# Performance work log

Measured on AMD Instinct MI355X. Metric: run time of the kernel, lower is better.

Reference implementation:

```python
import jax, jax.numpy as jnp
import numpy as np

ARITY, LABEL_DIM, H_DIM, B = 2, 128, 512, 16384
ARG_DIM = LABEL_DIM + ARITY * H_DIM


def setup_inputs() -> dict:
    key = jax.random.key(0)
    ks = jax.random.split(key, 12)
    s_lin = 1.0 / np.sqrt(ARG_DIM)
    inp = {
        "label": jax.random.normal(ks[0], (B, LABEL_DIM), jnp.float32),
        "children_h": jax.random.normal(ks[1], (ARITY, B, H_DIM), jnp.float32),
        "children_c": jax.random.normal(ks[2], (ARITY, B, H_DIM), jnp.float32),
        # torch Linear params: W (h, arg_dim), b (h,)
        "W_i": jax.random.normal(ks[3], (H_DIM, ARG_DIM), jnp.float32) * s_lin,
        "b_i": jax.random.normal(ks[4], (H_DIM,), jnp.float32) * s_lin,
        "W_o": jax.random.normal(ks[5], (H_DIM, ARG_DIM), jnp.float32) * s_lin,
        "b_o": jax.random.normal(ks[6], (H_DIM,), jnp.float32) * s_lin,
        "W_u": jax.random.normal(ks[7], (H_DIM, ARG_DIM), jnp.float32) * s_lin,
        "b_u": jax.random.normal(ks[8], (H_DIM,), jnp.float32) * s_lin,
        # forget params (xavier-ish init)
        "W_fl": jax.random.normal(ks[9], (H_DIM, LABEL_DIM), jnp.float32) * np.sqrt(2.0 / (H_DIM + LABEL_DIM)),
        "W_fs": jax.random.normal(ks[10], (ARITY, ARITY, H_DIM, H_DIM), jnp.float32) * np.sqrt(1.0 / H_DIM),
        "forget_bias": jax.random.normal(ks[11], (H_DIM,), jnp.float32) * 0.1,
    }
    return inp


def reference(label, children_h, children_c, W_i, b_i, W_o, b_o, W_u, b_u, W_fl, W_fs, forget_bias):
    arity, b, h = children_h.shape
    # x = cat([label, h_0, ..., h_{arity-1}], dim=1)  -> (B, arg_dim)
    x = jnp.concatenate([label, children_h.transpose(1, 0, 2).reshape(b, arity * h)], axis=1)
    i_gate = jax.nn.sigmoid(x @ W_i.T + b_i)
    o_gate = jax.nn.sigmoid(x @ W_o.T + b_o)
    u = jnp.tanh(x @ W_u.T + b_u)
    # per-child forget weight: [W_fl | W_fs[k,0] | ... | W_fs[k,arity-1]]  -> (arity, h, arg_dim)
    Wf = jnp.concatenate(
        [jnp.broadcast_to(W_fl, (arity,) + W_fl.shape),
         W_fs.transpose(0, 2, 1, 3).reshape(arity, h, arity * h)],
        axis=2,
    )
    # bmm (no bias inside sigmoid; forget_bias enters separately below)
    f = jax.nn.sigmoid(jnp.einsum("khd,bd->kbh", Wf, x))
    cells_composed = (f * children_c).sum(axis=0)          # (B, h)
    cells_forget_bias = forget_bias * children_c.sum(axis=0)
    next_cell = i_gate * u + cells_composed + cells_forget_bias
    out = jnp.tanh(o_gate * next_cell)
    return (next_cell, out)
```

## Files before the change

### kernel.cpp

```cpp
#include <hip/hip_runtime.h>
#include <hip/hip_bf16.h>
#include <cstdint>
#include <cstddef>

#define BROWS   16384
#define LDIM    128
#define HDIM    512
#define KDIM    1152
#define NGATES  2560

#define XB_BYTES  ((size_t)BROWS * KDIM * 2)
#define WB_BYTES  ((size_t)NGATES * KDIM * 2)

using f32x4   = __attribute__((ext_vector_type(4))) float;
using bfrag   = __attribute__((ext_vector_type(8))) short;

__device__ __forceinline__ short f2bf(float f) {
    union { float f; uint32_t u; } a; a.f = f;
    uint32_t u = a.u;
    uint32_t lsb = (u >> 16) & 1u;
    u += 0x7fffu + lsb;
    return (short)(u >> 16);
}
__device__ __forceinline__ float bf2f(short s) {
    union { uint32_t u; float f; } a;
    a.u = ((uint32_t)(uint16_t)s) << 16;
    return a.f;
}

__device__ __forceinline__ void load_lds16(const void* g, void* l) {
    __builtin_amdgcn_global_load_lds(
        (const __attribute__((address_space(1))) void*)g,
        (__attribute__((address_space(3))) void*)l, 16, 0, 0);
}

__device__ __forceinline__ float fast_sigmoid(float x) {
    return 1.0f / (1.0f + __expf(-x));
}
__device__ __forceinline__ float fast_tanh(float x) {
    float t = __expf(2.0f * x);
    return 1.0f - 2.0f / (t + 1.0f);
}

#define NBX  ((BROWS  * (KDIM / 8)) / 256)
#define NBW  ((NGATES * (KDIM / 8)) / 256)

__global__ __launch_bounds__(256) void pack_all(
    const float* __restrict__ label, const float* __restrict__ chh,
    const float* __restrict__ Wi, const float* __restrict__ Wo,
    const float* __restrict__ Wu, const float* __restrict__ Wfl,
    const float* __restrict__ Wfs,
    short* __restrict__ xb, short* __restrict__ Wb)
{
    const int perRow = KDIM / 8;
    int blk = blockIdx.x;
    const float* src;
    short* dst;
    if (blk < NBX) {
        int tid = blk * 256 + threadIdx.x;
        int b = tid / perRow;
        int d = (tid - b * perRow) * 8;
        if (d < LDIM) {
            src = label + (size_t)b * LDIM + d;
        } else {
            int dd = d - LDIM;
            int k  = dd >> 9;
            int j  = dd & 511;
            src = chh + ((size_t)k * BROWS + b) * HDIM + j;
        }
        dst = xb + (size_t)b * KDIM + d;
    } else {
        int tid = (blk - NBX) * 256 + threadIdx.x;
        int n = tid / perRow;
        int d = (tid - n * perRow) * 8;
        int g = n >> 9, h = n & 511;
        if (g == 0)      src = Wi + (size_t)h * KDIM + d;
        else if (g == 1) src = Wo + (size_t)h * KDIM + d;
        else if (g == 2) src = Wu + (size_t)h * KDIM + d;
        else {
            int k = g - 3;
            if (d < LDIM) {
                src = Wfl + (size_t)h * LDIM + d;
            } else {
                int dd = d - LDIM;
                int j  = dd >> 9;
                int jj = dd & 511;
                src = Wfs + (((size_t)(k * 2 + j) * HDIM + h) * HDIM) + jj;
            }
        }
        dst = Wb + (size_t)n * KDIM + d;
    }
    float4 v0 = *(const float4*)src;
    float4 v1 = *(const float4*)(src + 4);
    bfrag s;
    s[0] = f2bf(v0.x); s[1] = f2bf(v0.y); s[2] = f2bf(v0.z); s[3] = f2bf(v0.w);
    s[4] = f2bf(v1.x); s[5] = f2bf(v1.y); s[6] = f2bf(v1.z); s[7] = f2bf(v1.w);
    *(bfrag*)dst = s;
}

__global__ __launch_bounds__(256, 4) void gemm_bt(const short* __restrict__ A,
                                                  const short* __restrict__ Bt,
                                                  short* __restrict__ C) {
    __shared__ short As[128 * 32];
    __shared__ short Bs[128 * 32];

    const int t    = threadIdx.x;
    const int lane = t & 63;
    const int wave = t >> 6;
    const int wr   = wave >> 1;
    const int wc   = wave & 1;
    const int quad = lane >> 4;
    const int l16  = lane & 15;

    const int mBase = blockIdx.x * 128;
    const int nBase = blockIdx.y * 128;

    f32x4 acc[4][4] = {};

    const int s0 = t, s1 = t + 256;
    const int r0 = s0 >> 2, c0 = ((s0 & 3) ^ (r0 & 3)) * 8;
    const int r1 = s1 >> 2, c1 = ((s1 & 3) ^ (r1 & 3)) * 8;

    const short* Arow0 = A + (size_t)(mBase + r0) * KDIM + c0;
    const short* Arow1 = A + (size_t)(mBase + r1) * KDIM + c1;
    const short* Brow0 = Bt + (size_t)(nBase + r0) * KDIM + c0;
    const short* Brow1 = Bt + (size_t)(nBase + r1) * KDIM + c1;

    int aOff[4], bOff[4];
#pragma unroll
    for (int i = 0; i < 4; ++i) {
        int rowA = wr * 64 + i * 16 + l16;
        aOff[i] = rowA * 32 + ((quad ^ (rowA & 3)) * 8);
        int rowB = wc * 64 + i * 16 + l16;
        bOff[i] = rowB * 32 + ((quad ^ (rowB & 3)) * 8);
    }

    for (int k0 = 0; k0 < KDIM; k0 += 32) {
        load_lds16(Arow0 + k0, As + s0 * 8);
        load_lds16(Arow1 + k0, As + s1 * 8);
        load_lds16(Brow0 + k0, Bs + s0 * 8);
        load_lds16(Brow1 + k0, Bs + s1 * 8);
        __syncthreads();

        bfrag a[4], b[4];
#pragma unroll
        for (int i = 0; i < 4; ++i) {
            a[i] = *(const bfrag*)(As + aOff[i]);
            b[i] = *(const bfrag*)(Bs + bOff[i]);
        }
#pragma unroll
        for (int i = 0; i < 4; ++i)
#pragma unroll
            for (int j = 0; j < 4; ++j)
                acc[i][j] = __builtin_amdgcn_mfma_f32_16x16x32_bf16(a[i], b[j], acc[i][j], 0, 0, 0);
        __syncthreads();
    }

#pragma unroll
    for (int i = 0; i < 4; ++i) {
        int m0 = mBase + wr * 64 + i * 16 + quad * 4;
#pragma unroll
        for (int j = 0; j < 4; ++j) {
            int n = nBase + wc * 64 + j * 16 + l16;
#pragma unroll
            for (int r = 0; r < 4; ++r) {
                C[(size_t)(m0 + r) * NGATES + n] = f2bf(acc[i][j][r]);
            }
        }
    }
}

__global__ __launch_bounds__(256) void epilogue(const short* __restrict__ gates,
                                                const float* __restrict__ chc,
                                                const float* __restrict__ b_i,
                                                const float* __restrict__ b_o,
                                                const float* __restrict__ b_u,
                                                const float* __restrict__ fbias,
                                                float* __restrict__ out) {
    int tid = blockIdx.x * 256 + threadIdx.x;
    int b  = tid >> 6;
    int h8 = (tid & 63) << 3;

    const short* g = gates + (size_t)b * NGATES + h8;
    bfrag vi  = *(const bfrag*)(g);
    bfrag vo  = *(const bfrag*)(g + HDIM);
    bfrag vu  = *(const bfrag*)(g + 2 * HDIM);
    bfrag vf0 = *(const bfrag*)(g + 3 * HDIM);
    bfrag vf1 = *(const bfrag*)(g + 4 * HDIM);

    float4 bi0 = *(const float4*)(b_i + h8),   bi1 = *(const float4*)(b_i + h8 + 4);
    float4 bo0 = *(const float4*)(b_o + h8),   bo1 = *(const float4*)(b_o + h8 + 4);
    float4 bu0 = *(const float4*)(b_u + h8),   bu1 = *(const float4*)(b_u + h8 + 4);
    float4 fb0 = *(const float4*)(fbias + h8), fb1 = *(const float4*)(fbias + h8 + 4);

    size_t cbase = (size_t)b * HDIM + h8;
    float4 c00 = *(const float4*)(chc + cbase);
    float4 c01 = *(const float4*)(chc + cbase + 4);
    float4 c10 = *(const float4*)(chc + (size_t)BROWS * HDIM + cbase);
    float4 c11 = *(const float4*)(chc + (size_t)BROWS * HDIM + cbase + 4);

    float bi[8] = {bi0.x,bi0.y,bi0.z,bi0.w, bi1.x,bi1.y,bi1.z,bi1.w};
    float bo[8] = {bo0.x,bo0.y,bo0.z,bo0.w, bo1.x,bo1.y,bo1.z,bo1.w};
    float bu[8] = {bu0.x,bu0.y,bu0.z,bu0.w, bu1.x,bu1.y,bu1.z,bu1.w};
    float fb[8] = {fb0.x,fb0.y,fb0.z,fb0.w, fb1.x,fb1.y,fb1.z,fb1.w};
    float c0[8] = {c00.x,c00.y,c00.z,c00.w, c01.x,c01.y,c01.z,c01.w};
    float c1[8] = {c10.x,c10.y,c10.z,c10.w, c11.x,c11.y,c11.z,c11.w};

    float nc[8], ou[8];
#pragma unroll
    for (int e = 0; e < 8; ++e) {
        float ig = fast_sigmoid(bf2f(vi[e]) + bi[e]);
        float og = fast_sigmoid(bf2f(vo[e]) + bo[e]);
        float uu = fast_tanh(bf2f(vu[e]) + bu[e]);
        float f0 = fast_sigmoid(bf2f(vf0[e]));
        float f1 = fast_sigmoid(bf2f(vf1[e]));
        float ncell = ig * uu + f0 * c0[e] + f1 * c1[e] + fb[e] * (c0[e] + c1[e]);
        nc[e] = ncell;
        ou[e] = fast_tanh(og * ncell);
    }
    float4 n0 = {nc[0], nc[1], nc[2], nc[3]}, n1 = {nc[4], nc[5], nc[6], nc[7]};
    float4 o0 = {ou[0], ou[1], ou[2], ou[3]}, o1 = {ou[4], ou[5], ou[6], ou[7]};
    *(float4*)(out + cbase)     = n0;
    *(float4*)(out + cbase + 4) = n1;
    *(float4*)(out + (size_t)BROWS * HDIM + cbase)     = o0;
    *(float4*)(out + (size_t)BROWS * HDIM + cbase + 4) = o1;
}

extern "C" void kernel_launch(void* const* d_in, const int* in_sizes, int n_in,
                              void* d_out, int out_size, void* d_ws, size_t ws_size,
                              hipStream_t stream) {
    const float* label = (const float*)d_in[0];
    const float* chh   = (const float*)d_in[1];
    const float* chc   = (const float*)d_in[2];
    const float* W_i   = (const float*)d_in[3];
    const float* b_i   = (const float*)d_in[4];
    const float* W_o   = (const float*)d_in[5];
    const float* b_o   = (const float*)d_in[6];
    const float* W_u   = (const float*)d_in[7];
    const float* b_u   = (const float*)d_in[8];
    const float* W_fl  = (const float*)d_in[9];
    const float* W_fs  = (const float*)d_in[10];
    const float* fbias = (const float*)d_in[11];
    float* out = (float*)d_out;

    char* ws = (char*)d_ws;
    short* xb    = (short*)ws;
    short* Wb    = (short*)(ws + XB_BYTES);
    short* gates = (short*)(ws + XB_BYTES + WB_BYTES);

    pack_all<<<NBX + NBW, 256, 0, stream>>>(label, chh, W_i, W_o, W_u, W_fl, W_fs, xb, Wb);

    dim3 ggrid(BROWS / 128, NGATES / 128);
    gemm_bt<<<ggrid, 256, 0, stream>>>(xb, Wb, gates);

    epilogue<<<(BROWS * (HDIM / 8)) / 256, 256, 0, stream>>>(gates, chc, b_i, b_o, b_u, fbias, out);
}
```

Baseline: 333.0 us.

## Restructure GEMM into 256x256 tiles with double-buffered LDS and phased MFMA schedule

```diff
diff --git a/kernel.cpp b/kernel.cpp
--- a/kernel.cpp
+++ b/kernel.cpp
@@ -8,6 +8,7 @@
 #define HDIM    512
 #define KDIM    1152
 #define NGATES  2560
+#define NKT     (KDIM / 64)
 
 #define XB_BYTES  ((size_t)BROWS * KDIM * 2)
 #define WB_BYTES  ((size_t)NGATES * KDIM * 2)
@@ -98,76 +99,133 @@
     *(bfrag*)dst = s;
 }
 
-__global__ __launch_bounds__(256, 4) void gemm_bt(const short* __restrict__ A,
+__global__ __launch_bounds__(512, 2) void gemm_bt(const short* __restrict__ A,
                                                   const short* __restrict__ Bt,
                                                   short* __restrict__ C) {
-    __shared__ short As[128 * 32];
-    __shared__ short Bs[128 * 32];
+    __shared__ short As[2][16384];
+    __shared__ short Bs[2][16384];
 
     const int t    = threadIdx.x;
     const int lane = t & 63;
     const int wave = t >> 6;
-    const int wr   = wave >> 1;
-    const int wc   = wave & 1;
+    const int wr   = wave >> 2;
+    const int wc   = wave & 3;
     const int quad = lane >> 4;
     const int l16  = lane & 15;
 
-    const int mBase = blockIdx.x * 128;
-    const int nBase = blockIdx.y * 128;
-
-    f32x4 acc[4][4] = {};
-
-    const int s0 = t, s1 = t + 256;
-    const int r0 = s0 >> 2, c0 = ((s0 & 3) ^ (r0 & 3)) * 8;
-    const int r1 = s1 >> 2, c1 = ((s1 & 3) ^ (r1 & 3)) * 8;
-
-    const short* Arow0 = A + (size_t)(mBase + r0) * KDIM + c0;
-    const short* Arow1 = A + (size_t)(mBase + r1) * KDIM + c1;
-    const short* Brow0 = Bt + (size_t)(nBase + r0) * KDIM + c0;
-    const short* Brow1 = Bt + (size_t)(nBase + r1) * KDIM + c1;
-
-    int aOff[4], bOff[4];
+    const int swz   = (blockIdx.x & 7) * 80 + (blockIdx.x >> 3);
+    const int mBase = (swz & 63) * 256;
+    const int nBase = (swz >> 6) * 256;
+
+    f32x4 acc[8][4] = {};
+
+    const int sr  = t >> 3;
+    const int ssl = (t & 7) ^ (sr & 7);
+    const short* aSrc = A  + (size_t)(mBase + sr) * KDIM + ssl * 8;
+    const short* bSrc = Bt + (size_t)(nBase + sr) * KDIM + ssl * 8;
+    short* aDst = &As[0][0] + t * 8;
+    short* bDst = &Bs[0][0] + t * 8;
+
+#define STAGE_A(q, kt, buf) load_lds16(aSrc + (size_t)(q) * (64 * KDIM) + (kt) * 64, \
+                                       aDst + (buf) * 16384 + (q) * 4096)
+#define STAGE_B(q, kt, buf) load_lds16(bSrc + (size_t)(q) * (64 * KDIM) + (kt) * 64, \
+                                       bDst + (buf) * 16384 + (q) * 4096)
+
+    const int kswz0 = ((quad)     ^ (l16 & 7)) << 4;
+    const int kswz1 = ((quad + 4) ^ (l16 & 7)) << 4;
+    const int aRowB = (wr * 128 + l16) << 7;
+    const int bRowB = (wc * 64  + l16) << 7;
+
+#define DS_A(buf, mh, j, ks) (*(const bfrag*)((const char*)(&As[(buf)][0]) + aRowB + \
+                              (mh) * 8192 + (j) * 2048 + ((ks) ? kswz1 : kswz0)))
+#define DS_B(buf, nh, j, ks) (*(const bfrag*)((const char*)(&Bs[(buf)][0]) + bRowB + \
+                              (nh) * 4096 + (j) * 2048 + ((ks) ? kswz1 : kswz0)))
+
+#define MM(af, bfr, mi, ni) acc[mi][ni] = \
+    __builtin_amdgcn_mfma_f32_16x16x32_bf16(af, bfr, acc[mi][ni], 0, 0, 0)
+
+#define PHASE(buf, mh, nh, ...) do { \
+    bfrag a00 = DS_A(buf, mh, 0, 0), a01 = DS_A(buf, mh, 0, 1); \
+    bfrag a10 = DS_A(buf, mh, 1, 0), a11 = DS_A(buf, mh, 1, 1); \
+    bfrag a20 = DS_A(buf, mh, 2, 0), a21 = DS_A(buf, mh, 2, 1); \
+    bfrag a30 = DS_A(buf, mh, 3, 0), a31 = DS_A(buf, mh, 3, 1); \
+    bfrag b00 = DS_B(buf, nh, 0, 0), b01 = DS_B(buf, nh, 0, 1); \
+    bfrag b10 = DS_B(buf, nh, 1, 0), b11 = DS_B(buf, nh, 1, 1); \
+    __VA_ARGS__; \
+    __builtin_amdgcn_s_barrier(); \
+    asm volatile("s_waitcnt lgkmcnt(0)" ::: "memory"); \
+    __builtin_amdgcn_s_setprio(1); \
+    MM(a00, b00, (mh)*4+0, (nh)*2+0); \
+    MM(a10, b00, (mh)*4+1, (nh)*2+0); \
+    MM(a20, b00, (mh)*4+2, (nh)*2+0); \
+    MM(a30, b00, (mh)*4+3, (nh)*2+0); \
+    MM(a00, b10, (mh)*4+0, (nh)*2+1); \
+    MM(a10, b10, (mh)*4+1, (nh)*2+1); \
+    MM(a20, b10, (mh)*4+2, (nh)*2+1); \
+    MM(a30, b10, (mh)*4+3, (nh)*2+1); \
+    MM(a01, b01, (mh)*4+0, (nh)*2+0); \
+    MM(a11, b01, (mh)*4+1, (nh)*2+0); \
+    MM(a21, b01, (mh)*4+2, (nh)*2+0); \
+    MM(a31, b01, (mh)*4+3, (nh)*2+0); \
+    MM(a01, b11, (mh)*4+0, (nh)*2+1); \
+    MM(a11, b11, (mh)*4+1, (nh)*2+1); \
+    MM(a21, b11, (mh)*4+2, (nh)*2+1); \
+    MM(a31, b11, (mh)*4+3, (nh)*2+1); \
+    __builtin_amdgcn_s_setprio(0); \
+} while (0)
+
+    STAGE_A(0, 0, 0); STAGE_A(1, 0, 0); STAGE_A(2, 0, 0); STAGE_A(3, 0, 0);
+    STAGE_B(0, 0, 0); STAGE_B(1, 0, 0); STAGE_B(2, 0, 0); STAGE_B(3, 0, 0);
+    STAGE_A(0, 1, 1); STAGE_A(2, 1, 1);
+    asm volatile("s_waitcnt vmcnt(2)" ::: "memory");
+    __builtin_amdgcn_s_barrier();
+
+#pragma unroll 1
+    for (int k2 = 0; k2 < NKT / 2; ++k2) {
+        const int kt   = 2 * k2;
+        const bool more = (k2 < NKT / 2 - 1);
+
+        PHASE(0, 0, 0, STAGE_A(1, kt + 1, 1); STAGE_B(0, kt + 1, 1); STAGE_B(1, kt + 1, 1));
+        __builtin_amdgcn_s_barrier();
+        PHASE(0, 0, 1, STAGE_A(3, kt + 1, 1); STAGE_B(2, kt + 1, 1); STAGE_B(3, kt + 1, 1));
+        __builtin_amdgcn_s_barrier();
+        PHASE(0, 1, 0, if (more) STAGE_A(0, kt + 2, 0));
+        __builtin_amdgcn_s_barrier();
+        PHASE(0, 1, 1, if (more) STAGE_A(2, kt + 2, 0));
+        if (more) { asm volatile("s_waitcnt vmcnt(2)" ::: "memory"); }
+        else      { asm volatile("s_waitcnt vmcnt(0)" ::: "memory"); }
+        __builtin_amdgcn_s_barrier();
+
+        PHASE(1, 0, 0, if (more) { STAGE_A(1, kt + 2, 0); STAGE_B(0, kt + 2, 0); STAGE_B(1, kt + 2, 0); });
+        __builtin_amdgcn_s_barrier();
+        PHASE(1, 0, 1, if (more) { STAGE_A(3, kt + 2, 0); STAGE_B(2, kt + 2, 0); STAGE_B(3, kt + 2, 0); });
+        __builtin_amdgcn_s_barrier();
+        PHASE(1, 1, 0, if (more) STAGE_A(0, kt + 3, 1));
+        __builtin_amdgcn_s_barrier();
+        PHASE(1, 1, 1, if (more) STAGE_A(2, kt + 3, 1));
+        if (more) { asm volatile("s_waitcnt vmcnt(2)" ::: "memory"); }
+        else      { asm volatile("s_waitcnt vmcnt(0)" ::: "memory"); }
+        __builtin_amdgcn_s_barrier();
+    }
+
 #pragma unroll
-    for (int i = 0; i < 4; ++i) {
-        int rowA = wr * 64 + i * 16 + l16;
-        aOff[i] = rowA * 32 + ((quad ^ (rowA & 3)) * 8);
-        int rowB = wc * 64 + i * 16 + l16;
-        bOff[i] = rowB * 32 + ((quad ^ (rowB & 3)) * 8);
-    }
-
-    for (int k0 = 0; k0 < KDIM; k0 += 32) {
-        load_lds16(Arow0 + k0, As + s0 * 8);
-        load_lds16(Arow1 + k0, As + s1 * 8);
-        load_lds16(Brow0 + k0, Bs + s0 * 8);
-        load_lds16(Brow1 + k0, Bs + s1 * 8);
-        __syncthreads();
-
-        bfrag a[4], b[4];
+    for (int mi = 0; mi < 8; ++mi) {
+        const int row0 = mBase + wr * 128 + mi * 16 + quad * 4;
 #pragma unroll
-        for (int i = 0; i < 4; ++i) {
-            a[i] = *(const bfrag*)(As + aOff[i]);
-            b[i] = *(const bfrag*)(Bs + bOff[i]);
-        }
-#pragma unroll
-        for (int i = 0; i < 4; ++i)
-#pragma unroll
-            for (int j = 0; j < 4; ++j)
-                acc[i][j] = __builtin_amdgcn_mfma_f32_16x16x32_bf16(a[i], b[j], acc[i][j], 0, 0, 0);
-        __syncthreads();
-    }
-
-#pragma unroll
-    for (int i = 0; i < 4; ++i) {
-        int m0 = mBase + wr * 64 + i * 16 + quad * 4;
-#pragma unroll
-        for (int j = 0; j < 4; ++j) {
-            int n = nBase + wc * 64 + j * 16 + l16;
+        for (int ni = 0; ni < 4; ++ni) {
+            const int col = nBase + wc * 64 + ni * 16 + l16;
 #pragma unroll
             for (int r = 0; r < 4; ++r) {
-                C[(size_t)(m0 + r) * NGATES + n] = f2bf(acc[i][j][r]);
+                C[(size_t)(row0 + r) * NGATES + col] = f2bf(acc[mi][ni][r]);
             }
         }
     }
+#undef PHASE
+#undef MM
+#undef DS_A
+#undef DS_B
+#undef STAGE_A
+#undef STAGE_B
 }
 
 __global__ __launch_bounds__(256) void epilogue(const short* __restrict__ gates,
@@ -250,8 +308,7 @@
 
     pack_all<<<NBX + NBW, 256, 0, stream>>>(label, chh, W_i, W_o, W_u, W_fl, W_fs, xb, Wb);
 
-    dim3 ggrid(BROWS / 128, NGATES / 128);
-    gemm_bt<<<ggrid, 256, 0, stream>>>(xb, Wb, gates);
+    gemm_bt<<<dim3(640), 512, 0, stream>>>(xb, Wb, gates);
 
     epilogue<<<(BROWS * (HDIM / 8)) / 256, 256, 0, stream>>>(gates, chc, b_i, b_o, b_u, fbias, out);
 }
```

Measured after the change: 351.5 us. 5.6% more time.
